# Performance work log

Hardware: AMD Instinct MI355X
Metric: run time of the kernel (lower is better)

Reference implementation:

```python
import jax, jax.numpy as jnp
import numpy as np

N_NODES = 100000
N_EDGES = 1600000
IN_CH = 64
HID = 64
N_GRAPHS = 64


def _sage_conv(x, src, dst, Wl, bl, Wr, n_nodes):
    # PyG SAGEConv (aggr='mean'): out = lin_l(mean_{j in N(i)} x_j) + lin_r(x_i)
    msg = x[src]                                            # [E, d] gather
    agg = jax.ops.segment_sum(msg, dst, num_segments=n_nodes)
    cnt = jax.ops.segment_sum(jnp.ones((src.shape[0],), x.dtype), dst,
                              num_segments=n_nodes)
    agg = agg / jnp.maximum(cnt, 1.0)[:, None]
    return agg @ Wl + bl + x @ Wr


def setup_inputs() -> dict:
    key = jax.random.key(0)
    ks = jax.random.split(key, 16)
    x = jax.random.normal(ks[0], (N_NODES, IN_CH), jnp.float32)
    edge_index = jax.random.randint(ks[1], (2, N_EDGES), 0, N_NODES, jnp.int64)
    batch = jnp.sort(jax.random.randint(ks[2], (N_NODES,), 0, N_GRAPHS, jnp.int64))

    def glorot(k, fan_in, fan_out):
        s = jnp.sqrt(2.0 / (fan_in + fan_out))
        return jax.random.normal(k, (fan_in, fan_out), jnp.float32) * s

    params = {
        'W1l': glorot(ks[3], IN_CH, HID), 'b1': jnp.zeros((HID,), jnp.float32),
        'W1r': glorot(ks[4], IN_CH, HID),
        'W2l': glorot(ks[5], HID, HID), 'b2': jnp.zeros((HID,), jnp.float32),
        'W2r': glorot(ks[6], HID, HID),
        'W3l': glorot(ks[7], HID, HID), 'b3': jnp.zeros((HID,), jnp.float32),
        'W3r': glorot(ks[8], HID, HID),
        'Wc1': glorot(ks[9], HID, HID // 2), 'bc1': jnp.zeros((HID // 2,), jnp.float32),
        'Wc2': glorot(ks[10], HID // 2, 2), 'bc2': jnp.zeros((2,), jnp.float32),
    }
    return {'x': x, 'edge_index': edge_index, 'batch': batch, **params}


def reference(x, edge_index, batch,
              W1l, b1, W1r, W2l, b2, W2r, W3l, b3, W3r,
              Wc1, bc1, Wc2, bc2):
    src, dst = edge_index[0], edge_index[1]
    n = x.shape[0]
    h = jax.nn.relu(_sage_conv(x, src, dst, W1l, b1, W1r, n))   # dropout = identity (eval)
    h = jax.nn.relu(_sage_conv(h, src, dst, W2l, b2, W2r, n))
    h = jax.nn.relu(_sage_conv(h, src, dst, W3l, b3, W3r, n))
    # global mean pool over graphs
    sums = jax.ops.segment_sum(h, batch, num_segments=N_GRAPHS)
    cnts = jax.ops.segment_sum(jnp.ones((n,), h.dtype), batch, num_segments=N_GRAPHS)
    g = sums / jnp.maximum(cnts, 1.0)[:, None]                  # [G, HID]
    # MLP head (dropout = identity at eval)
    return jax.nn.relu(g @ Wc1 + bc1) @ Wc2 + bc2               # [G, 2]
```

## Files before the change

### kernel.cpp

```cpp
#include <hip/hip_runtime.h>
#include <hip/hip_bf16.h>
#include <hip/hip_fp16.h>

typedef unsigned int u32;
typedef unsigned short u16;
typedef _Float16 f16x8 __attribute__((ext_vector_type(8)));
typedef float f32x4 __attribute__((ext_vector_type(4)));

#define NBLK1 512
#define CVTBLK 256
#define WPREP 6

__device__ __forceinline__ u16 f2h(float f) { return __half_as_ushort(__float2half(f)); }
__device__ __forceinline__ u32 packh2(float a, float b) {
    return (u32)f2h(a) | ((u32)f2h(b) << 16);
}

__device__ __forceinline__ int gidx(const void* p, long long i, int w64) {
    if (w64) return (int)((const long long*)p)[i];
    return ((const int*)p)[i];
}

__device__ __forceinline__ int detect_w64(const int* edge_words, int E, int tid, int* sh) {
    if (tid == 0) *sh = 0;
    __syncthreads();
    const long long totalWords = 2LL * E;
    const long long step = totalWords / 256;
    long long w = ((long long)tid * step) | 1;
    int nz = (w < totalWords) ? edge_words[w] : 0;
    if (nz) atomicOr(sh, 1);
    __syncthreads();
    return (*sh) ? 0 : 1;
}

__global__ void __launch_bounds__(256) fused_hist_cvt(
        const void* __restrict__ edge, int* __restrict__ flag, u32* __restrict__ ticket,
        u32* __restrict__ HG, int E, int n, int nb1,
        const float* __restrict__ X, u16* __restrict__ Xh,
        const float* __restrict__ W1l, const float* __restrict__ W1r,
        const float* __restrict__ W2l, const float* __restrict__ W2r,
        const float* __restrict__ W3l, const float* __restrict__ W3r,
        _Float16* __restrict__ WFrag) {
    const int tid = threadIdx.x;
    if (blockIdx.x < NBLK1) {
        __shared__ u32 h[256];
        __shared__ int shnz;
        h[tid] = 0;
        const int w64 = detect_w64((const int*)edge, E, tid, &shnz);
        if (blockIdx.x == 0 && tid == 0) { flag[0] = w64; ticket[0] = 0; }
        __syncthreads();
        const int chunk = (E + NBLK1 - 1) / NBLK1;
        const int s = blockIdx.x * chunk;
        const int e = min(s + chunk, E);
        for (int i = s + tid; i < e; i += 256) {
            int d = gidx(edge, (long long)E + i, w64);
            if ((unsigned)d >= (unsigned)n) d = 0;
            atomicAdd(&h[d >> 9], 1);
        }
        __syncthreads();
        for (int b = tid; b < nb1; b += 256) HG[b * NBLK1 + blockIdx.x] = h[b];
        return;
    }
    if (blockIdx.x >= NBLK1 + CVTBLK) {
        const int b = blockIdx.x - NBLK1 - CVTBLK;
        const float* Ws[WPREP] = {W1l, W1r, W2l, W2r, W3l, W3r};
        const float* src = Ws[b];
        _Float16* dst = WFrag + b * 4096;
        for (int idx = tid; idx < 4096; idx += 256) {
            const int k = idx >> 6, c = idx & 63;
            const int d = ((((k >> 5) * 4 + ((k >> 3) & 3)) * 4 + (c >> 4)) * 16 + (c & 15)) * 8
                          + (k & 7);
            dst[d] = (_Float16)src[idx];
        }
        return;
    }
    const long long total4 = (long long)n * 16;
    const long long stride = (long long)CVTBLK * 256;
    long long i = (long long)(blockIdx.x - NBLK1) * 256 + tid;
    const float4* X4 = (const float4*)X;
    uint2* O = (uint2*)Xh;
    for (; i < total4; i += stride) {
        float4 v = X4[i];
        uint2 o;
        o.x = packh2(v.x, v.y);
        o.y = packh2(v.z, v.w);
        O[i] = o;
    }
}

__global__ void scanAB(u32* __restrict__ HG, u32* __restrict__ blockSums,
                       u32* __restrict__ SB, u32* __restrict__ ticket, int n) {
    __shared__ u32 ts[256];
    __shared__ int isLast;
    const int ITEMS = 8;
    const int tid = threadIdx.x;
    int base = blockIdx.x * 2048 + tid * ITEMS;
    u32 v[ITEMS];
    u32 sum = 0;
#pragma unroll
    for (int i = 0; i < ITEMS; ++i) {
        int idx = base + i;
        v[i] = (idx < n) ? HG[idx] : 0;
        sum += v[i];
    }
    ts[tid] = sum;
    __syncthreads();
    u32 incl = sum;
    for (int d = 1; d < 256; d <<= 1) {
        u32 y = 0;
        if (tid >= d) y = ts[tid - d];
        __syncthreads();
        incl += y;
        ts[tid] = incl;
        __syncthreads();
    }
    u32 run = incl - sum;
#pragma unroll
    for (int i = 0; i < ITEMS; ++i) {
        int idx = base + i;
        if (idx < n) HG[idx] = run;
        run += v[i];
    }
    if (tid == 255) {
        atomicExch(&blockSums[blockIdx.x], incl);
        __threadfence();
        u32 t = atomicAdd(&ticket[0], 1u);
        isLast = (t == gridDim.x - 1);
    }
    __syncthreads();
    if (!isLast) return;
    const int nb = gridDim.x;
    u32 bv = (tid < nb) ? atomicAdd(&blockSums[tid], 0u) : 0;
    ts[tid] = bv;
    __syncthreads();
    u32 bincl = bv;
    for (int d = 1; d < 256; d <<= 1) {
        u32 y = 0;
        if (tid >= d) y = ts[tid - d];
        __syncthreads();
        bincl += y;
        ts[tid] = bincl;
        __syncthreads();
    }
    if (tid < nb) SB[tid] = bincl - bv;
}

__global__ void __launch_bounds__(256) p1_scatter(const void* __restrict__ edge,
                                                  const int* __restrict__ flag,
                                                  const u32* __restrict__ HG,
                                                  const u32* __restrict__ SB,
                                                  u32* __restrict__ P, int E, int n, int nb1) {
    __shared__ u32 base[256];
    __shared__ u32 cur[256];
    const int tid = threadIdx.x;
    cur[tid] = 0;
    for (int b = tid; b < nb1; b += 256) {
        int i = b * NBLK1 + blockIdx.x;
        base[b] = HG[i] + SB[i >> 11];
    }
    __syncthreads();
    const int w64 = flag[0];
    const int chunk = (E + NBLK1 - 1) / NBLK1;
    const int s = blockIdx.x * chunk;
    const int e = min(s + chunk, E);
    for (int i = s + tid; i < e; i += 256) {
        int d = gidx(edge, (long long)E + i, w64);
        if ((unsigned)d >= (unsigned)n) d = 0;
        int sv = gidx(edge, i, w64);
        if ((unsigned)sv >= (unsigned)n) sv = 0;
        const int b1 = d >> 9;
        u32 r = atomicAdd(&cur[b1], 1);
        P[base[b1] + r] = (u32)sv | ((u32)(d & 511) << 17);
    }
}

__global__ void __launch_bounds__(512) p2_kernel(const u32* __restrict__ P,
                                                 const u32* __restrict__ HG,
                                                 const u32* __restrict__ SB,
                                                 u32* __restrict__ offs,
                                                 int* __restrict__ ss,
                                                 float* __restrict__ pool,
                                                 int E, int n, int nb1) {
    __shared__ u32 h2[512];
    __shared__ u32 ts[512];
    const int tid = threadIdx.x;
    const int b = blockIdx.x;
    if (b == 0)
        for (int i = tid; i < 4096; i += 512) pool[i] = 0.f;
    const int i0 = b * NBLK1;
    const int bs = (int)(HG[i0] + SB[i0 >> 11]);
    int be;
    if (b + 1 < nb1) {
        const int i1 = (b + 1) * NBLK1;
        be = (int)(HG[i1] + SB[i1 >> 11]);
    } else be = E;
    h2[tid] = 0;
    __syncthreads();
    for (int i = bs + tid; i < be; i += 512) atomicAdd(&h2[(P[i] >> 17) & 511], 1);
    __syncthreads();
    u32 v = h2[tid];
    ts[tid] = v;
    __syncthreads();
    u32 incl = v;
    for (int d = 1; d < 512; d <<= 1) {
        u32 y = 0;
        if (tid >= d) y = ts[tid - d];
        __syncthreads();
        incl += y;
        ts[tid] = incl;
        __syncthreads();
    }
    u32 run = incl - v;
    h2[tid] = run;
    const int node0 = b * 512 + tid;
    if (node0 < n) offs[node0] = bs + run;
    if (b == 0 && tid == 0) offs[n] = (u32)E;
    __syncthreads();
    for (int i = bs + tid; i < be; i += 512) {
        u32 p = P[i];
        u32 r = atomicAdd(&h2[(p >> 17) & 511], 1);
        ss[bs + r] = (int)(p & 0x1FFFFu);
    }
}

__global__ void __launch_bounds__(256) sage3(
        const u16* __restrict__ G, const u32* __restrict__ offs,
        const int* __restrict__ ss,
        const _Float16* __restrict__ WF,
        const float* __restrict__ Bv,
        u16* __restrict__ Hout, float* __restrict__ pool,
        const void* __restrict__ batch, const int* __restrict__ flag,
        int n, int mode) {
    const int tid = threadIdx.x;
    const int lane = tid & 63;
    const int quad = lane >> 4;
    const int m16 = lane & 15;
    const int w64 = mode ? flag[0] : 0;
    const _Float16* wlp = WF + quad * 512 + m16 * 8;
    const _Float16* wrp = wlp + 4096;
    const float btv[4] = {Bv[m16], Bv[16 + m16], Bv[32 + m16], Bv[48 + m16]};

    const int ntiles = (n + 15) >> 4;
    const int nwaves = gridDim.x * 4;
    for (int tile = blockIdx.x * 4 + (tid >> 6); tile < ntiles; tile += nwaves) {
        const int nodeBase = tile << 4;
        const int node_m = nodeBase + m16;
        const int nodeA = node_m < n ? node_m : n - 1;
        const u32 o0 = offs[nodeA];
        const int deg = node_m < n ? (int)(offs[nodeA + 1] - o0) : 0;
        const int* sp = ss + o0;
        f16x8 s0, s1;
#pragma unroll
        for (int j = 0; j < 8; ++j) { s0[j] = (_Float16)0; s1[j] = (_Float16)0; }
        int e = 0;
        for (; e + 4 <= deg; e += 4) {
            const int iA = sp[e], iB = sp[e + 1], iC = sp[e + 2], iD = sp[e + 3];
            const f16x8* pA = (const f16x8*)(G + ((size_t)iA << 6)) + quad;
            const f16x8* pB = (const f16x8*)(G + ((size_t)iB << 6)) + quad;
            const f16x8* pC = (const f16x8*)(G + ((size_t)iC << 6)) + quad;
            const f16x8* pD = (const f16x8*)(G + ((size_t)iD << 6)) + quad;
            f16x8 a0 = pA[0], a1 = pA[4];
            f16x8 b0 = pB[0], b1 = pB[4];
            f16x8 c0 = pC[0], c1 = pC[4];
            f16x8 d0 = pD[0], d1 = pD[4];
            s0 += a0; s1 += a1;
            s0 += b0; s1 += b1;
            s0 += c0; s1 += c1;
            s0 += d0; s1 += d1;
        }
        for (; e < deg; ++e) {
            const f16x8* pA = (const f16x8*)(G + ((size_t)(sp[e]) << 6)) + quad;
            s0 += pA[0]; s1 += pA[4];
        }
        const float rdf = deg > 0 ? 1.f / (float)deg : 0.f;
        const _Float16 hrd = (_Float16)rdf;
#pragma unroll
        for (int j = 0; j < 8; ++j) { s0[j] *= hrd; s1[j] *= hrd; }
        const f16x8 as0 = *(const f16x8*)(G + (size_t)nodeA * 64 + quad * 8);
        const f16x8 as1 = *(const f16x8*)(G + (size_t)nodeA * 64 + 32 + quad * 8);
#pragma unroll
        for (int t = 0; t < 4; ++t) {
            const f16x8 l0 = *(const f16x8*)(wlp + t * 128);
            const f16x8 l1 = *(const f16x8*)(wlp + 2048 + t * 128);
            const f16x8 r0 = *(const f16x8*)(wrp + t * 128);
            const f16x8 r1 = *(const f16x8*)(wrp + 2048 + t * 128);
            const float bt = btv[t];
            f32x4 acc = {bt, bt, bt, bt};
            acc = __builtin_amdgcn_mfma_f32_16x16x32_f16(s0, l0, acc, 0, 0, 0);
            acc = __builtin_amdgcn_mfma_f32_16x16x32_f16(s1, l1, acc, 0, 0, 0);
            acc = __builtin_amdgcn_mfma_f32_16x16x32_f16(as0, r0, acc, 0, 0, 0);
            acc = __builtin_amdgcn_mfma_f32_16x16x32_f16(as1, r1, acc, 0, 0, 0);
            if (mode == 0) {
#pragma unroll
                for (int rg = 0; rg < 4; ++rg) {
                    const int node = nodeBase + quad * 4 + rg;
                    if (node < n)
                        Hout[(size_t)node * 64 + t * 16 + m16] = f2h(fmaxf(acc[rg], 0.f));
                }
            } else {
                float v0 = fmaxf(acc[0], 0.f), v1 = fmaxf(acc[1], 0.f);
                float v2 = fmaxf(acc[2], 0.f), v3 = fmaxf(acc[3], 0.f);
                const int lastN = nodeBase + 15 < n ? nodeBase + 15 : n - 1;
                const int g0 = gidx(batch, nodeBase, w64) & 63;
                const int g1 = gidx(batch, lastN, w64) & 63;
                if (nodeBase + 15 < n && g0 == g1) {
                    float cs = v0 + v1 + v2 + v3;
                    cs += __shfl_xor(cs, 16, 64);
                    cs += __shfl_xor(cs, 32, 64);
                    if (quad == 0) atomicAdd(&pool[g0 * 64 + t * 16 + m16], cs);
                } else {
                    const float vv[4] = {v0, v1, v2, v3};
#pragma unroll
                    for (int rg = 0; rg < 4; ++rg) {
                        const int node = nodeBase + quad * 4 + rg;
                        if (node < n) {
                            const int g = gidx(batch, node, w64) & 63;
                            atomicAdd(&pool[g * 64 + t * 16 + m16], vv[rg]);
                        }
                    }
                }
            }
        }
    }
}

__global__ void head_kernel(const float* __restrict__ pool, const void* __restrict__ batch,
                            const int* __restrict__ flag,
                            const float* __restrict__ Wc1, const float* __restrict__ bc1,
                            const float* __restrict__ Wc2, const float* __restrict__ bc2,
                            float* __restrict__ out, int n) {
    __shared__ float gm[64 * 64];
    __shared__ float am[64 * 32];
    __shared__ int cnts[64];
    const int tid = threadIdx.x;
    const int w64 = flag[0];
    if (tid < 64) {
        int lo = 0, hi = n;
        while (lo < hi) { int mid = (lo + hi) >> 1; if (gidx(batch, mid, w64) < tid) lo = mid + 1; else hi = mid; }
        int lo2 = 0, hi2 = n;
        int v2 = tid + 1;
        while (lo2 < hi2) { int mid = (lo2 + hi2) >> 1; if (gidx(batch, mid, w64) < v2) lo2 = mid + 1; else hi2 = mid; }
        cnts[tid] = lo2 - lo;
    }
    __syncthreads();
    for (int i = tid; i < 4096; i += 256) {
        int g = i >> 6;
        float c = (float)(cnts[g] > 0 ? cnts[g] : 1);
        gm[i] = pool[i] / c;
    }
    __syncthreads();
    for (int i = tid; i < 64 * 32; i += 256) {
        int g = i >> 5, j = i & 31;
        float acc = bc1[j];
        for (int k = 0; k < 64; ++k) acc += gm[g * 64 + k] * Wc1[k * 32 + j];
        am[i] = acc > 0.f ? acc : 0.f;
    }
    __syncthreads();
    if (tid < 128) {
        int g = tid >> 1, o = tid & 1;
        float acc = bc2[o];
        for (int j = 0; j < 32; ++j) acc += am[g * 32 + j] * Wc2[j * 2 + o];
        out[tid] = acc;
    }
}

extern "C" void kernel_launch(void* const* d_in, const int* in_sizes, int n_in,
                              void* d_out, int out_size, void* d_ws, size_t ws_size,
                              hipStream_t stream) {
    const float* x   = (const float*)d_in[0];
    const void* edge = d_in[1];
    const void* batch = d_in[2];
    const float* W1l = (const float*)d_in[3];
    const float* b1  = (const float*)d_in[4];
    const float* W1r = (const float*)d_in[5];
    const float* W2l = (const float*)d_in[6];
    const float* b2  = (const float*)d_in[7];
    const float* W2r = (const float*)d_in[8];
    const float* W3l = (const float*)d_in[9];
    const float* b3  = (const float*)d_in[10];
    const float* W3r = (const float*)d_in[11];
    const float* Wc1 = (const float*)d_in[12];
    const float* bc1 = (const float*)d_in[13];
    const float* Wc2 = (const float*)d_in[14];
    const float* bc2 = (const float*)d_in[15];

    const int n = in_sizes[0] / 64;
    const int E = in_sizes[1] / 2;
    const int nb1 = (n + 511) >> 9;
    const int NS = nb1 * NBLK1;

    char* w = (char*)d_ws;
    size_t o = 0;
    auto take = [&](size_t bytes) -> void* {
        void* p = w + o;
        o = (o + bytes + 511) & ~(size_t)511;
        return p;
    };
    int* flag      = (int*)take(sizeof(int));
    u32* ticket    = (u32*)take(2 * sizeof(u32));
    u32* offs      = (u32*)take((size_t)(n + 1) * sizeof(u32));
    u32* HG        = (u32*)take((size_t)(NS + 1) * sizeof(u32));
    u32* blockSums = (u32*)take(256 * sizeof(u32));
    u32* SB        = (u32*)take(256 * sizeof(u32));
    u32* P         = (u32*)take((size_t)E * sizeof(u32));
    int* ss        = (int*)take((size_t)E * sizeof(int));
    u16* Xh        = (u16*)take((size_t)n * 64 * sizeof(u16));
    u16* HA        = (u16*)take((size_t)n * 64 * sizeof(u16));
    u16* HB        = (u16*)take((size_t)n * 64 * sizeof(u16));
    _Float16* WF   = (_Float16*)take(WPREP * 4096 * sizeof(_Float16));
    float* pool    = (float*)take(64 * 64 * sizeof(float));

    fused_hist_cvt<<<NBLK1 + CVTBLK + WPREP, 256, 0, stream>>>(
        edge, flag, ticket, HG, E, n, nb1, x, Xh, W1l, W1r, W2l, W2r, W3l, W3r, WF);
    const int nbScan = (NS + 2047) / 2048;
    scanAB<<<nbScan, 256, 0, stream>>>(HG, blockSums, SB, ticket, NS);
    p1_scatter<<<NBLK1, 256, 0, stream>>>(edge, flag, HG, SB, P, E, n, nb1);
    p2_kernel<<<nb1, 512, 0, stream>>>(P, HG, SB, offs, ss, pool, E, n, nb1);

    const int ntiles = (n + 15) >> 4;
    const int SLBLK = (ntiles + 3) >> 2;
    sage3<<<SLBLK, 256, 0, stream>>>(Xh, offs, ss, WF, b1, HA, nullptr,
                                     batch, flag, n, 0);
    sage3<<<SLBLK, 256, 0, stream>>>(HA, offs, ss, WF + 2 * 4096, b2, HB, nullptr,
                                     batch, flag, n, 0);
    sage3<<<SLBLK, 256, 0, stream>>>(HB, offs, ss, WF + 4 * 4096, b3, nullptr, pool,
                                     batch, flag, n, 1);
    head_kernel<<<1, 256, 0, stream>>>(pool, batch, flag, Wc1, bc1, Wc2, bc2,
                                       (float*)d_out, n);
}
```

Measured before the change: 294.8 us.

## Split each SAGE tile's channels across two waves and exchange via LDS

Each 16-node tile is now processed by two waves, each gathering half of the 64 channels (one 16-byte load per neighbour instead of two), which doubles the waves in flight for the latency-bound neighbour gather. The halves are exchanged through shared memory with a block barrier, and each wave computes half of the output columns with MFMA. This adds an LDS round trip, two __syncthreads per tile, and imbalance when the two tiles in a block differ in degree.

```diff
diff --git a/kernel.cpp b/kernel.cpp
--- a/kernel.cpp
+++ b/kernel.cpp
@@ -223,7 +223,7 @@
     }
 }
 
-__global__ void __launch_bounds__(256) sage3(
+__global__ void __launch_bounds__(256) sage4(
         const u16* __restrict__ G, const u32* __restrict__ offs,
         const int* __restrict__ ss,
         const _Float16* __restrict__ WF,
@@ -231,96 +231,106 @@
         u16* __restrict__ Hout, float* __restrict__ pool,
         const void* __restrict__ batch, const int* __restrict__ flag,
         int n, int mode) {
-    const int tid = threadIdx.x;
+    __shared__ _Float16 XL[2][16][72];
+    const int tid = threadIdx.x;
+    const int wv = tid >> 6;
+    const int tIdx = wv >> 1;
+    const int half = wv & 1;
     const int lane = tid & 63;
     const int quad = lane >> 4;
     const int m16 = lane & 15;
+    const int cb = half * 32 + quad * 8;
     const int w64 = mode ? flag[0] : 0;
-    const _Float16* wlp = WF + quad * 512 + m16 * 8;
-    const _Float16* wrp = wlp + 4096;
-    const float btv[4] = {Bv[m16], Bv[16 + m16], Bv[32 + m16], Bv[48 + m16]};
 
     const int ntiles = (n + 15) >> 4;
-    const int nwaves = gridDim.x * 4;
-    for (int tile = blockIdx.x * 4 + (tid >> 6); tile < ntiles; tile += nwaves) {
+    const int npairs = (ntiles + 1) >> 1;
+    for (int pair = blockIdx.x; pair < npairs; pair += gridDim.x) {
+        const int tile = pair * 2 + tIdx;
+        const int tvalid = tile < ntiles;
         const int nodeBase = tile << 4;
         const int node_m = nodeBase + m16;
-        const int nodeA = node_m < n ? node_m : n - 1;
+        const int valid = tvalid && node_m < n;
+        const int nodeA = valid ? node_m : n - 1;
         const u32 o0 = offs[nodeA];
-        const int deg = node_m < n ? (int)(offs[nodeA + 1] - o0) : 0;
+        const int deg = valid ? (int)(offs[nodeA + 1] - o0) : 0;
         const int* sp = ss + o0;
-        f16x8 s0, s1;
-#pragma unroll
-        for (int j = 0; j < 8; ++j) { s0[j] = (_Float16)0; s1[j] = (_Float16)0; }
+        f16x8 s;
+#pragma unroll
+        for (int j = 0; j < 8; ++j) s[j] = (_Float16)0;
         int e = 0;
         for (; e + 4 <= deg; e += 4) {
             const int iA = sp[e], iB = sp[e + 1], iC = sp[e + 2], iD = sp[e + 3];
-            const f16x8* pA = (const f16x8*)(G + ((size_t)iA << 6)) + quad;
-            const f16x8* pB = (const f16x8*)(G + ((size_t)iB << 6)) + quad;
-            const f16x8* pC = (const f16x8*)(G + ((size_t)iC << 6)) + quad;
-            const f16x8* pD = (const f16x8*)(G + ((size_t)iD << 6)) + quad;
-            f16x8 a0 = pA[0], a1 = pA[4];
-            f16x8 b0 = pB[0], b1 = pB[4];
-            f16x8 c0 = pC[0], c1 = pC[4];
-            f16x8 d0 = pD[0], d1 = pD[4];
-            s0 += a0; s1 += a1;
-            s0 += b0; s1 += b1;
-            s0 += c0; s1 += c1;
-            s0 += d0; s1 += d1;
+            f16x8 a = *(const f16x8*)(G + ((size_t)iA << 6) + cb);
+            f16x8 b = *(const f16x8*)(G + ((size_t)iB << 6) + cb);
+            f16x8 c = *(const f16x8*)(G + ((size_t)iC << 6) + cb);
+            f16x8 d = *(const f16x8*)(G + ((size_t)iD << 6) + cb);
+            s += a; s += b; s += c; s += d;
         }
-        for (; e < deg; ++e) {
-            const f16x8* pA = (const f16x8*)(G + ((size_t)(sp[e]) << 6)) + quad;
-            s0 += pA[0]; s1 += pA[4];
-        }
+        for (; e < deg; ++e)
+            s += *(const f16x8*)(G + ((size_t)(sp[e]) << 6) + cb);
         const float rdf = deg > 0 ? 1.f / (float)deg : 0.f;
         const _Float16 hrd = (_Float16)rdf;
 #pragma unroll
-        for (int j = 0; j < 8; ++j) { s0[j] *= hrd; s1[j] *= hrd; }
-        const f16x8 as0 = *(const f16x8*)(G + (size_t)nodeA * 64 + quad * 8);
-        const f16x8 as1 = *(const f16x8*)(G + (size_t)nodeA * 64 + 32 + quad * 8);
-#pragma unroll
-        for (int t = 0; t < 4; ++t) {
-            const f16x8 l0 = *(const f16x8*)(wlp + t * 128);
-            const f16x8 l1 = *(const f16x8*)(wlp + 2048 + t * 128);
-            const f16x8 r0 = *(const f16x8*)(wrp + t * 128);
-            const f16x8 r1 = *(const f16x8*)(wrp + 2048 + t * 128);
-            const float bt = btv[t];
-            f32x4 acc = {bt, bt, bt, bt};
-            acc = __builtin_amdgcn_mfma_f32_16x16x32_f16(s0, l0, acc, 0, 0, 0);
-            acc = __builtin_amdgcn_mfma_f32_16x16x32_f16(s1, l1, acc, 0, 0, 0);
-            acc = __builtin_amdgcn_mfma_f32_16x16x32_f16(as0, r0, acc, 0, 0, 0);
-            acc = __builtin_amdgcn_mfma_f32_16x16x32_f16(as1, r1, acc, 0, 0, 0);
-            if (mode == 0) {
-#pragma unroll
-                for (int rg = 0; rg < 4; ++rg) {
-                    const int node = nodeBase + quad * 4 + rg;
-                    if (node < n)
-                        Hout[(size_t)node * 64 + t * 16 + m16] = f2h(fmaxf(acc[rg], 0.f));
-                }
-            } else {
-                float v0 = fmaxf(acc[0], 0.f), v1 = fmaxf(acc[1], 0.f);
-                float v2 = fmaxf(acc[2], 0.f), v3 = fmaxf(acc[3], 0.f);
-                const int lastN = nodeBase + 15 < n ? nodeBase + 15 : n - 1;
-                const int g0 = gidx(batch, nodeBase, w64) & 63;
-                const int g1 = gidx(batch, lastN, w64) & 63;
-                if (nodeBase + 15 < n && g0 == g1) {
-                    float cs = v0 + v1 + v2 + v3;
-                    cs += __shfl_xor(cs, 16, 64);
-                    cs += __shfl_xor(cs, 32, 64);
-                    if (quad == 0) atomicAdd(&pool[g0 * 64 + t * 16 + m16], cs);
-                } else {
-                    const float vv[4] = {v0, v1, v2, v3};
+        for (int j = 0; j < 8; ++j) s[j] *= hrd;
+        *(f16x8*)(&XL[tIdx][m16][cb]) = s;
+        __syncthreads();
+        int zz;
+        asm volatile("v_mov_b32 %0, 0" : "=v"(zz));
+        const f16x8 soth = *(const f16x8*)(&XL[tIdx][m16][(half ^ 1) * 32 + quad * 8]);
+        const f16x8 s0 = half ? soth : s;
+        const f16x8 s1 = half ? s : soth;
+        if (tvalid) {
+            const _Float16* wlp = WF + zz + quad * 512 + m16 * 8;
+            const _Float16* wrp = wlp + 4096;
+            const u16* gs = G + ((size_t)nodeA << 6) + zz;
+            const f16x8 as0 = *(const f16x8*)(gs + quad * 8);
+            const f16x8 as1 = *(const f16x8*)(gs + 32 + quad * 8);
+#pragma unroll 1
+            for (int tt = 0; tt < 2; ++tt) {
+                const int t = half * 2 + tt;
+                const f16x8 l0 = *(const f16x8*)(wlp + t * 128);
+                const f16x8 l1 = *(const f16x8*)(wlp + 2048 + t * 128);
+                const f16x8 r0 = *(const f16x8*)(wrp + t * 128);
+                const f16x8 r1 = *(const f16x8*)(wrp + 2048 + t * 128);
+                const float bt = Bv[t * 16 + m16];
+                f32x4 acc = {bt, bt, bt, bt};
+                acc = __builtin_amdgcn_mfma_f32_16x16x32_f16(s0, l0, acc, 0, 0, 0);
+                acc = __builtin_amdgcn_mfma_f32_16x16x32_f16(s1, l1, acc, 0, 0, 0);
+                acc = __builtin_amdgcn_mfma_f32_16x16x32_f16(as0, r0, acc, 0, 0, 0);
+                acc = __builtin_amdgcn_mfma_f32_16x16x32_f16(as1, r1, acc, 0, 0, 0);
+                if (mode == 0) {
 #pragma unroll
                     for (int rg = 0; rg < 4; ++rg) {
                         const int node = nodeBase + quad * 4 + rg;
-                        if (node < n) {
-                            const int g = gidx(batch, node, w64) & 63;
-                            atomicAdd(&pool[g * 64 + t * 16 + m16], vv[rg]);
+                        if (node < n)
+                            Hout[(size_t)node * 64 + t * 16 + m16] = f2h(fmaxf(acc[rg], 0.f));
+                    }
+                } else {
+                    float v0 = fmaxf(acc[0], 0.f), v1 = fmaxf(acc[1], 0.f);
+                    float v2 = fmaxf(acc[2], 0.f), v3 = fmaxf(acc[3], 0.f);
+                    const int lastN = nodeBase + 15 < n ? nodeBase + 15 : n - 1;
+                    const int g0 = gidx(batch, nodeBase, w64) & 63;
+                    const int g1 = gidx(batch, lastN, w64) & 63;
+                    if (nodeBase + 15 < n && g0 == g1) {
+                        float cs = v0 + v1 + v2 + v3;
+                        cs += __shfl_xor(cs, 16, 64);
+                        cs += __shfl_xor(cs, 32, 64);
+                        if (quad == 0) atomicAdd(&pool[g0 * 64 + t * 16 + m16], cs);
+                    } else {
+                        const float vv[4] = {v0, v1, v2, v3};
+#pragma unroll
+                        for (int rg = 0; rg < 4; ++rg) {
+                            const int node = nodeBase + quad * 4 + rg;
+                            if (node < n) {
+                                const int g = gidx(batch, node, w64) & 63;
+                                atomicAdd(&pool[g * 64 + t * 16 + m16], vv[rg]);
+                            }
                         }
                     }
                 }
             }
         }
+        __syncthreads();
     }
 }
 
@@ -418,13 +428,13 @@
     p2_kernel<<<nb1, 512, 0, stream>>>(P, HG, SB, offs, ss, pool, E, n, nb1);
 
     const int ntiles = (n + 15) >> 4;
-    const int SLBLK = (ntiles + 3) >> 2;
-    sage3<<<SLBLK, 256, 0, stream>>>(Xh, offs, ss, WF, b1, HA, nullptr,
-                                     batch, flag, n, 0);
-    sage3<<<SLBLK, 256, 0, stream>>>(HA, offs, ss, WF + 2 * 4096, b2, HB, nullptr,
-                                     batch, flag, n, 0);
-    sage3<<<SLBLK, 256, 0, stream>>>(HB, offs, ss, WF + 4 * 4096, b3, nullptr, pool,
-                                     batch, flag, n, 1);
+    const int npairs = (ntiles + 1) >> 1;
+    sage4<<<npairs, 256, 0, stream>>>(Xh, offs, ss, WF, b1, HA, nullptr,
+                                      batch, flag, n, 0);
+    sage4<<<npairs, 256, 0, stream>>>(HA, offs, ss, WF + 2 * 4096, b2, HB, nullptr,
+                                      batch, flag, n, 0);
+    sage4<<<npairs, 256, 0, stream>>>(HB, offs, ss, WF + 4 * 4096, b3, nullptr, pool,
+                                      batch, flag, n, 1);
     head_kernel<<<1, 256, 0, stream>>>(pool, batch, flag, Wc1, bc1, Wc2, bc2,
                                        (float*)d_out, n);
 }
```

New measurement: 302.8 us. 1.03x slower.
